# Optimization experiments

Measured on AMD Instinct MI355X. Metric: run time of the kernel, lower is better.

## Reference

```python
import jax, jax.numpy as jnp
import numpy as np
from jax import lax

B_, T_, E_, H_, V_ = 8, 128, 256, 512, 32000


def setup_inputs() -> dict:
    key = jax.random.key(0)
    ks = jax.random.split(key, 16)
    s = 0.05
    n = lambda k, shp: (jax.random.normal(k, shp, dtype=jnp.float32) * s)
    return {
        "tokens": jax.random.randint(ks[0], (B_, T_), 0, V_),
        "TASK": 0,
        "embed_table": n(ks[1], (V_, E_)),
        # shared LSTM (PyTorch gate order i,f,g,o packed along 4H)
        "Wih_s": n(ks[2], (E_, 4 * H_)),
        "Whh_s": n(ks[3], (H_, 4 * H_)),
        "b_s": n(ks[4], (4 * H_,)),
        # task attention projections
        "Ws_w": n(ks[5], (E_ + 2 * H_, H_)),
        "Ws_b": n(ks[6], (H_,)),
        "Us_w": n(ks[7], (H_, 1)),
        "Us_b": n(ks[8], (1,)),
        # task-specific message LSTM cell (extra message path Rt)
        "Wih_t": n(ks[9], (E_, 4 * H_)),
        "Whh_t": n(ks[10], (H_, 4 * H_)),
        "Wmh_t": n(ks[11], (H_, 4 * H_)),
        "b_t": n(ks[12], (4 * H_,)),
    }


def _gates(pre, c):
    i, f, g, o = jnp.split(pre, 4, axis=-1)
    c_new = jax.nn.sigmoid(f) * c + jax.nn.sigmoid(i) * jnp.tanh(g)
    h_new = jax.nn.sigmoid(o) * jnp.tanh(c_new)
    return h_new, c_new


def _forward(tokens, TASK, embed_table, Wih_s, Whh_s, b_s,
             Ws_w, Ws_b, Us_w, Us_b, Wih_t, Whh_t, Wmh_t, b_t):
    B, T = tokens.shape
    H = Whh_s.shape[0]
    emb = embed_table[tokens]                     # [B,T,E]
    emb_t = jnp.transpose(emb, (1, 0, 2))         # [T,B,E]
    zeros = jnp.zeros((B, H), dtype=emb.dtype)

    # shared single-layer LSTM over time
    def shared_cell(carry, x_t):
        h, c = carry
        h, c = _gates(x_t @ Wih_s + h @ Whh_s + b_s, c)
        return (h, c), h

    (h_last, _), shared_out_t = lax.scan(shared_cell, (zeros, zeros), emb_t)
    shared_out = jnp.transpose(shared_out_t, (1, 0, 2))   # [B,T,H]
    h_shared = h_last[:, None, :]                         # [B,1,H]

    # task-specific attention-weighted message LSTM
    def task_step(carry, x_t):
        h, c = carry
        h_task = jnp.broadcast_to(h[:, None, :], (B, T, H))
        catted = jnp.concatenate([shared_out, h_task, emb], axis=-1)  # [B,T,E+2H]
        a = jnp.tanh(catted @ Ws_w + Ws_b)                            # [B,T,H]
        Si = a @ Us_w + Us_b                                          # [B,T,1]
        Bw = jax.nn.softmax(Si, axis=1)                               # over time
        Rt = jnp.sum(Bw * h_shared, axis=1)                           # [B,H]
        h, c = _gates(x_t @ Wih_t + h @ Whh_t + Rt @ Wmh_t + b_t, c)
        return (h, c), h

    _, outs_t = lax.scan(task_step, (zeros, zeros), emb_t)
    return jnp.transpose(outs_t, (1, 0, 2))               # [B,T,H]


def reference(tokens, TASK, embed_table, Wih_s, Whh_s, b_s,
              Ws_w, Ws_b, Us_w, Us_b, Wih_t, Whh_t, Wmh_t, b_t):
    return _forward(tokens, TASK, embed_table, Wih_s, Whh_s, b_s,
                    Ws_w, Ws_b, Us_w, Us_b, Wih_t, Whh_t, Wmh_t, b_t)
```

## Files before the change

### kernel.cpp

```cpp
#include <hip/hip_runtime.h>
#include <math.h>

#define B_   8
#define T_   128
#define E_   256
#define H_   512
#define G_   2048
#define NWG  256
#define NTHR 512

typedef unsigned int u32;


__device__ __forceinline__ float sigf(float x) {
  return 1.0f / (1.0f + __expf(-x));
}
__device__ __forceinline__ float tanh_f(float x) {
  float xx = fminf(15.0f, fmaxf(-15.0f, x));
  float e  = __expf(2.0f * xx);
  return (e - 1.0f) / (e + 1.0f);
}

__device__ __forceinline__ unsigned short f2bf(float x) {
  u32 u = __float_as_uint(x);
  u += 0x7fffu + ((u >> 16) & 1u);
  return (unsigned short)(u >> 16);
}
__device__ __forceinline__ float bf2f(unsigned short s) {
  return __uint_as_float(((u32)s) << 16);
}

__global__ void init_ws(u32* w) {
  int i = blockIdx.x * blockDim.x + threadIdx.x;
  if (i < 4096)      w[i] = 0u;
  else if (i < 8192) w[i] = 1u;
}

__device__ __forceinline__ int wl_idx(int k, int c) { return k * 64 + (c ^ ((k >> 4) & 31)); }
__device__ __forceinline__ int xl_idx(int c, int t) { return c * T_ + (t ^ ((c & 31) << 1)); }

__device__ __forceinline__ void stage_W(const float* __restrict__ W, int rows,
                                        int s, float* __restrict__ Wl) {
  for (int idx = threadIdx.x; idx < rows * 64; idx += NTHR) {
    int k = idx >> 6, c = idx & 63;
    Wl[wl_idx(k, c)] = W[k * G_ + ((c >> 4) * H_ + s * 16 + (c & 15))];
  }
}

__attribute__((amdgpu_waves_per_eu(2)))
__global__ __launch_bounds__(NTHR, 1) void lstm_all(
    const int* __restrict__ tokens, const float* __restrict__ embed,
    const float* __restrict__ Wih_s, const float* __restrict__ Whh_s,
    const float* __restrict__ b_s,
    const float* __restrict__ Wih_t, const float* __restrict__ Whh_t,
    const float* __restrict__ Wmh_t, const float* __restrict__ b_t,
    float* __restrict__ out, u32* __restrict__ img) {
  __shared__ float Wl[H_ * 64];
  __shared__ unsigned short Xl[64 * T_];
  __shared__ float h_lds[H_];
  __shared__ float hOut[16];

  const int tid = threadIdx.x;
  const int l   = tid & 63;
  const int wv  = tid >> 6;
  const int b   = blockIdx.x & 7;
  const int s   = blockIdx.x >> 3;
  const int kch = l >> 3;
  const int cc  = ((l & 7) >> 1) * 16 + 2 * wv + (l & 1);
  const int d   = l & 1;
  const int bH  = b * H_;

  int wd = 1 << 20;
  float wreg[64];

  auto computeX = [&](const float* __restrict__ Wih, const float* __restrict__ bias) {
    stage_W(Wih, E_, s, Wl);
    __syncthreads();
    const int t = tid >> 2, grp = tid & 3;
    const int tok = tokens[b * T_ + t];
    const float4* er = (const float4*)(embed + (size_t)tok * E_);
    float acc[16];
#pragma unroll
    for (int j = 0; j < 16; ++j) acc[j] = bias[grp * H_ + s * 16 + j];
    for (int e4 = 0; e4 < E_ / 4; ++e4) {
      float4 em = er[e4];
#pragma unroll
      for (int eo = 0; eo < 4; ++eo) {
        float ev = reinterpret_cast<const float*>(&em)[eo];
        const int k = e4 * 4 + eo;
#pragma unroll
        for (int j = 0; j < 16; ++j) acc[j] += ev * Wl[wl_idx(k, grp * 16 + j)];
      }
    }
#pragma unroll
    for (int j = 0; j < 16; ++j) Xl[xl_idx(grp * 16 + j, t)] = f2bf(acc[j]);
  };

  auto load_wreg = [&] {
#pragma unroll
    for (int i = 0; i < 16; ++i) {
      const int q = (i + 2 * kch) & 15;
#pragma unroll
      for (int j = 0; j < 4; ++j)
        wreg[i * 4 + j] = Wl[wl_idx(kch * 64 + q * 4 + j, cc)];
    }
#pragma unroll
    for (int kk = 0; kk < 64; ++kk) asm volatile("" : "+v"(wreg[kk]));
  };

  auto poll_own = [&](unsigned gen) {
    const u32 par = (gen >> 1) & 1u;
    const u32* p = img + (gen & 1u) * 4096 + bH + tid;
    u32 u;
    for (;;) {
      u = __hip_atomic_load(p, __ATOMIC_RELAXED, __HIP_MEMORY_SCOPE_AGENT);
      if ((u & 1u) == par) break;
      if (--wd < 0) break;
      __builtin_amdgcn_s_sleep(1);
    }
    h_lds[tid] = __uint_as_float(u);
  };

  auto do_dot = [&]() -> float {
    float a0 = 0.f, a1 = 0.f, a2 = 0.f, a3 = 0.f;
    const float4* h4 = (const float4*)(h_lds + kch * 64);
#pragma unroll
    for (int i = 0; i < 16; ++i) {
      const int q = (i + 2 * kch) & 15;
      float4 hv = h4[q];
      a0 += hv.x * wreg[i * 4 + 0];
      a1 += hv.y * wreg[i * 4 + 1];
      a2 += hv.z * wreg[i * 4 + 2];
      a3 += hv.w * wreg[i * 4 + 3];
    }
    float sum = (a0 + a1) + (a2 + a3);
    sum += __shfl_xor(sum, 8);
    sum += __shfl_xor(sum, 16);
    sum += __shfl_xor(sum, 32);
    return sum;
  };

  computeX(Wih_s, b_s);
  __syncthreads();
  stage_W(Whh_s, H_, s, Wl);
  __syncthreads();
  load_wreg();

  float c_reg = 0.f, Mreg = 0.f;

  for (int t = 0; t < T_; ++t) {
    float pre = 0.f;
    if (t > 0) {
      poll_own((unsigned)t);
      __syncthreads();
      pre = do_dot();
    }
    if (l < 8) pre += bf2f(Xl[xl_idx(cc, t)]);
    float gi = __shfl(pre, d),     gf = __shfl(pre, 2 + d),
          gg = __shfl(pre, 4 + d), go = __shfl(pre, 6 + d);
    float cn = sigf(gf) * c_reg + sigf(gi) * tanh_f(gg);
    float hn = sigf(go) * tanh_f(cn);
    c_reg = cn;
    if (l < 2) hOut[2 * wv + l] = hn;
    __syncthreads();
    if (tid < 16) {
      const unsigned gw = (unsigned)t + 1u;
      u32 hb = (__float_as_uint(hOut[tid]) & ~1u) | ((gw >> 1) & 1u);
      __hip_atomic_store(img + (gw & 1u) * 4096 + bH + s * 16 + tid, hb,
                         __ATOMIC_RELAXED, __HIP_MEMORY_SCOPE_AGENT);
    }
  }

  __syncthreads();
  stage_W(Wmh_t, H_, s, Wl);
  __syncthreads();
  load_wreg();
  poll_own(128u);
  __syncthreads();
  Mreg = do_dot();

  __syncthreads();
  computeX(Wih_t, b_t);
  __syncthreads();
  stage_W(Whh_t, H_, s, Wl);
  __syncthreads();
  load_wreg();

  c_reg = 0.f;
  for (int t = 0; t < T_; ++t) {
    float pre = 0.f;
    if (t > 0) {
      poll_own(128u + (unsigned)t);
      __syncthreads();
      pre = do_dot();
    }
    if (l < 8) pre += bf2f(Xl[xl_idx(cc, t)]) + Mreg;
    float gi = __shfl(pre, d),     gf = __shfl(pre, 2 + d),
          gg = __shfl(pre, 4 + d), go = __shfl(pre, 6 + d);
    float cn = sigf(gf) * c_reg + sigf(gi) * tanh_f(gg);
    float hn = sigf(go) * tanh_f(cn);
    c_reg = cn;
    if (l < 2) hOut[2 * wv + l] = hn;
    __syncthreads();
    if (tid < 16) {
      if (t < T_ - 1) {
        const unsigned gw = 129u + (unsigned)t;
        u32 hb = (__float_as_uint(hOut[tid]) & ~1u) | ((gw >> 1) & 1u);
        __hip_atomic_store(img + (gw & 1u) * 4096 + bH + s * 16 + tid, hb,
                           __ATOMIC_RELAXED, __HIP_MEMORY_SCOPE_AGENT);
      }
      out[b * (T_ * H_) + t * H_ + s * 16 + tid] = hOut[tid];
    }
  }
}

extern "C" void kernel_launch(void* const* d_in, const int* in_sizes, int n_in,
                              void* d_out, int out_size, void* d_ws, size_t ws_size,
                              hipStream_t stream) {
  const int*   tokens = (const int*)d_in[0];
  const float* embed  = (const float*)d_in[2];
  const float* Wih_s  = (const float*)d_in[3];
  const float* Whh_s  = (const float*)d_in[4];
  const float* b_s    = (const float*)d_in[5];
  const float* Wih_t  = (const float*)d_in[10];
  const float* Whh_t  = (const float*)d_in[11];
  const float* Wmh_t  = (const float*)d_in[12];
  const float* b_t    = (const float*)d_in[13];
  float* out = (float*)d_out;
  u32*   img = (u32*)d_ws;

  hipLaunchKernelGGL(init_ws, dim3(8), dim3(1024), 0, stream, img);
  hipLaunchKernelGGL(lstm_all, dim3(NWG), dim3(NTHR), 0, stream,
                     tokens, embed, Wih_s, Whh_s, b_s,
                     Wih_t, Whh_t, Wmh_t, b_t, out, img);
}
```

Measured before the change: 656.5 us.

## Add XCD-local L2 fast path for cross-workgroup hidden-state exchange

Each workgroup records its XCD id, and each batch group of workgroups votes on whether all 32 members share one XCD. If they do, consumers spin on an L2-coherent copy of the published hidden state with sc0 loads, falling back to the device-scope (MALL) copy after repeated misses. Entries now carry a full 64-bit generation tag so stale values cannot be taken. The aim is lower latency per timestep barrier, at the cost of double stores, a startup vote, and dependence on workgroup-to-XCD placement, which may rarely put a whole group on one XCD.

```diff
diff --git a/kernel.cpp b/kernel.cpp
--- a/kernel.cpp
+++ b/kernel.cpp
@@ -10,6 +10,7 @@
 #define NTHR 512
 
 typedef unsigned int u32;
+typedef unsigned long long u64;
 
 
 __device__ __forceinline__ float sigf(float x) {
@@ -32,8 +33,7 @@
 
 __global__ void init_ws(u32* w) {
   int i = blockIdx.x * blockDim.x + threadIdx.x;
-  if (i < 4096)      w[i] = 0u;
-  else if (i < 8192) w[i] = 1u;
+  if (i < 33024) w[i] = 0xFFFFFFFFu;
 }
 
 __device__ __forceinline__ int wl_idx(int k, int c) { return k * 64 + (c ^ ((k >> 4) & 31)); }
@@ -54,11 +54,16 @@
     const float* __restrict__ b_s,
     const float* __restrict__ Wih_t, const float* __restrict__ Whh_t,
     const float* __restrict__ Wmh_t, const float* __restrict__ b_t,
-    float* __restrict__ out, u32* __restrict__ img) {
+    float* __restrict__ out, u64* __restrict__ ws) {
   __shared__ float Wl[H_ * 64];
   __shared__ unsigned short Xl[64 * T_];
   __shared__ float h_lds[H_];
   __shared__ float hOut[16];
+  __shared__ u32 flagLds;
+
+  u64* __restrict__ imgL2   = ws;
+  u64* __restrict__ imgMall = ws + 8192;
+  u32* __restrict__ tbl     = (u32*)(ws + 16384);
 
   const int tid = threadIdx.x;
   const int l   = tid & 63;
@@ -68,7 +73,30 @@
   const int kch = l >> 3;
   const int cc  = ((l & 7) >> 1) * 16 + 2 * wv + (l & 1);
   const int d   = l & 1;
-  const int bH  = b * H_;
+  const unsigned bH = (unsigned)(b * H_);
+
+  const u32 xcd = ((u32)__builtin_amdgcn_s_getreg(6164)) & 15u;
+  if (tid == 0)
+    __hip_atomic_store(tbl + blockIdx.x, xcd, __ATOMIC_RELAXED,
+                       __HIP_MEMORY_SCOPE_AGENT);
+  u32 vote = 1u;
+  if (tid < 32) {
+    int wd2 = 1 << 20;
+    u32 v;
+    for (;;) {
+      v = __hip_atomic_load(tbl + b + 8 * tid, __ATOMIC_RELAXED,
+                            __HIP_MEMORY_SCOPE_AGENT);
+      if (v != 0xFFFFFFFFu || --wd2 < 0) break;
+      __builtin_amdgcn_s_sleep(1);
+    }
+    vote = (v == xcd && wd2 >= 0) ? 1u : 0u;
+  }
+  if (tid < 64) {
+    unsigned long long bal = __ballot(vote != 0u);
+    if (tid == 0) flagLds = (bal == ~0ull) ? 1u : 0u;
+  }
+  __syncthreads();
+  int l2cnt = (flagLds != 0u) ? 6 : 0;
 
   int wd = 1 << 20;
   float wreg[64];
@@ -110,15 +138,41 @@
 
   auto poll_own = [&](unsigned gen) {
     const u32 par = (gen >> 1) & 1u;
-    const u32* p = img + (gen & 1u) * 4096 + bH + tid;
-    u32 u;
-    for (;;) {
-      u = __hip_atomic_load(p, __ATOMIC_RELAXED, __HIP_MEMORY_SCOPE_AGENT);
-      if ((u & 1u) == par) break;
-      if (--wd < 0) break;
-      __builtin_amdgcn_s_sleep(1);
-    }
-    h_lds[tid] = __uint_as_float(u);
+    const unsigned idx = (gen & 1u) * 4096u + bH + (unsigned)tid;
+    u32 val = 0u;
+    bool got = false;
+    if (l2cnt > 0) {
+      const u64* p = imgL2 + idx;
+      for (int i = 0; i < 96; ++i) {
+        u64 v;
+        asm volatile("global_load_dwordx2 %0, %1, off sc0\n\ts_waitcnt vmcnt(0)"
+                     : "=v"(v) : "v"(p) : "memory");
+        if ((u32)(v >> 32) == gen && (((u32)v) & 1u) == par) {
+          val = (u32)v; got = true; break;
+        }
+      }
+      l2cnt = got ? 6 : (l2cnt - 1);
+    }
+    if (!got) {
+      const u64* q = imgMall + idx;
+      for (;;) {
+        u64 v = __hip_atomic_load(q, __ATOMIC_RELAXED, __HIP_MEMORY_SCOPE_AGENT);
+        if ((u32)(v >> 32) == gen && (((u32)v) & 1u) == par) { val = (u32)v; break; }
+        if (--wd < 0) break;
+        __builtin_amdgcn_s_sleep(1);
+      }
+    }
+    h_lds[tid] = __uint_as_float(val);
+  };
+
+  auto publish = [&](unsigned gen, int fi, float hn) {
+    u32 v32 = (__float_as_uint(hn) & ~1u) | ((gen >> 1) & 1u);
+    u64 pack = ((u64)gen << 32) | (u64)v32;
+    const unsigned idx = (gen & 1u) * 4096u + bH + (unsigned)fi;
+    u64* p = imgL2 + idx;
+    asm volatile("global_store_dwordx2 %0, %1, off" :: "v"(p), "v"(pack) : "memory");
+    __hip_atomic_store(imgMall + idx, pack, __ATOMIC_RELAXED,
+                       __HIP_MEMORY_SCOPE_AGENT);
   };
 
   auto do_dot = [&]() -> float {
@@ -163,12 +217,8 @@
     c_reg = cn;
     if (l < 2) hOut[2 * wv + l] = hn;
     __syncthreads();
-    if (tid < 16) {
-      const unsigned gw = (unsigned)t + 1u;
-      u32 hb = (__float_as_uint(hOut[tid]) & ~1u) | ((gw >> 1) & 1u);
-      __hip_atomic_store(img + (gw & 1u) * 4096 + bH + s * 16 + tid, hb,
-                         __ATOMIC_RELAXED, __HIP_MEMORY_SCOPE_AGENT);
-    }
+    if (tid < 16)
+      publish((unsigned)t + 1u, s * 16 + tid, hOut[tid]);
   }
 
   __syncthreads();
@@ -203,12 +253,8 @@
     if (l < 2) hOut[2 * wv + l] = hn;
     __syncthreads();
     if (tid < 16) {
-      if (t < T_ - 1) {
-        const unsigned gw = 129u + (unsigned)t;
-        u32 hb = (__float_as_uint(hOut[tid]) & ~1u) | ((gw >> 1) & 1u);
-        __hip_atomic_store(img + (gw & 1u) * 4096 + bH + s * 16 + tid, hb,
-                           __ATOMIC_RELAXED, __HIP_MEMORY_SCOPE_AGENT);
-      }
+      if (t < T_ - 1)
+        publish(129u + (unsigned)t, s * 16 + tid, hOut[tid]);
       out[b * (T_ * H_) + t * H_ + s * 16 + tid] = hOut[tid];
     }
   }
@@ -227,10 +273,9 @@
   const float* Wmh_t  = (const float*)d_in[12];
   const float* b_t    = (const float*)d_in[13];
   float* out = (float*)d_out;
-  u32*   img = (u32*)d_ws;
-
-  hipLaunchKernelGGL(init_ws, dim3(8), dim3(1024), 0, stream, img);
+
+  hipLaunchKernelGGL(init_ws, dim3(33), dim3(1024), 0, stream, (u32*)d_ws);
   hipLaunchKernelGGL(lstm_all, dim3(NWG), dim3(NTHR), 0, stream,
                      tokens, embed, Wih_s, Whh_s, b_s,
-                     Wih_t, Whh_t, Wmh_t, b_t, out, img);
-}
+                     Wih_t, Whh_t, Wmh_t, b_t, out, (u64*)d_ws);
+}
```

Measured after the change: 771.7 us. 17.5% more time.
